# Performance work log

Measured on AMD Instinct MI355X. Metric: run time of the kernel, lower is better.

## Reference

```python
import jax, jax.numpy as jnp
import numpy as np

B, S, D = 1024, 60, 256   # seq_len=60 is hard-coded by nn.Linear(dim*60, n_experts)
H = 1024                  # d_inner
E = 8                     # n_experts
TOPK = 2
CAP = B * TOPK // E       # balanced per-expert capacity = 256


def setup_inputs() -> dict:
    key = jax.random.key(0)
    ks = jax.random.split(key, 9)
    s = 0.02
    return {
        "x":        jax.random.normal(ks[0], (B, S, D), dtype=jnp.float32),
        "W_switch": jax.random.normal(ks[1], (S * D, E), dtype=jnp.float32) * s,
        "b_switch": jnp.zeros((E,), dtype=jnp.float32),
        "W1":       jax.random.normal(ks[2], (E, D, H), dtype=jnp.float32) * s,
        "b1":       jnp.zeros((E, H), dtype=jnp.float32),
        "W2":       jax.random.normal(ks[3], (E, H, D), dtype=jnp.float32) * s,
        "b2":       jnp.zeros((E, D), dtype=jnp.float32),
        "gamma":    jnp.ones((D,), dtype=jnp.float32),
        "beta":     jnp.zeros((D,), dtype=jnp.float32),
    }


def reference(x, W_switch, b_switch, W1, b1, W2, b2, gamma, beta):
    # --- routing: softmax over experts per batch element ---
    logits = x.reshape(B, S * D) @ W_switch + b_switch          # [B, E]
    probs = jax.nn.softmax(logits, axis=-1)
    # balanced dispatch: each expert takes its top-CAP batch indices
    _, idx = jax.lax.top_k(probs.T, CAP)                        # [E, CAP] int32
    xe = x[idx]                                                 # gather -> [E, CAP, S, D]
    # --- per-expert grouped GEMMs (Column- then Row-parallel linear) ---
    h = jax.nn.gelu(jnp.einsum('ecsd,edh->ecsh', xe, W1)
                    + b1[:, None, None, :], approximate=False)  # [E, CAP, S, H]
    oe = jnp.einsum('ecsh,ehd->ecsd', h, W2) + b2[:, None, None, :]  # [E, CAP, S, D]
    # --- scatter-combine via index_add over the batch dim ---
    out = jnp.zeros_like(x).at[idx.reshape(-1)].add(oe.reshape(E * CAP, S, D))
    # --- residual + post-LayerNorm (pre_lnorm=False) ---
    z = x + out
    mu = jnp.mean(z, axis=-1, keepdims=True)
    var = jnp.var(z, axis=-1, keepdims=True)
    return (z - mu) * jax.lax.rsqrt(var + 1e-5) * gamma + beta
```

## Files before the change

kernel.cpp:

```cpp
#include <hip/hip_runtime.h>
#include <hip/hip_bf16.h>
#include <math.h>

#define NB   1024
#define NS   60
#define ND   256
#define NH   1024
#define NE   8
#define NCAP 256
#define NTOK (NCAP*NS)
#define BM   64
#define NBLK (NTOK/BM)
#define A_PAD 264
#define P_PAD 136

typedef __attribute__((ext_vector_type(8))) short  short8;
typedef __attribute__((ext_vector_type(4))) float  floatx4;

__device__ __forceinline__ unsigned short f2bf(float f) {
    union { float f; unsigned u; } cv; cv.f = f;
    unsigned u = cv.u;
    u += 0x7FFFu + ((u >> 16) & 1u);
    return (unsigned short)(u >> 16);
}

__global__ void k_prep_x(const float* __restrict__ x, unsigned short* __restrict__ xb,
                         float* __restrict__ acc, int n4) {
    int i = blockIdx.x * blockDim.x + threadIdx.x;
    if (i >= n4) return;
    float4 v = ((const float4*)x)[i];
    ((float4*)acc)[i] = v;
    ushort4 o;
    o.x = f2bf(v.x); o.y = f2bf(v.y); o.z = f2bf(v.z); o.w = f2bf(v.w);
    ((ushort4*)xb)[i] = o;
}

__global__ void k_pack_w1(const float* __restrict__ W1, unsigned short* __restrict__ W1b) {
    int tid = blockIdx.x * blockDim.x + threadIdx.x;
    int lane = tid & 63;
    int f = tid >> 6;
    int kt  = f & 7;
    int hnt = (f >> 3) & 63;
    int e   = f >> 9;
    int n = hnt * 16 + (lane & 15);
    int k = kt * 32 + (lane >> 4) * 8;
    const float* src = W1 + ((size_t)(e * 256 + k)) * 1024 + n;
    ushort4 a, b;
    a.x = f2bf(src[0 * 1024]); a.y = f2bf(src[1 * 1024]);
    a.z = f2bf(src[2 * 1024]); a.w = f2bf(src[3 * 1024]);
    b.x = f2bf(src[4 * 1024]); b.y = f2bf(src[5 * 1024]);
    b.z = f2bf(src[6 * 1024]); b.w = f2bf(src[7 * 1024]);
    ((ushort4*)W1b)[tid * 2]     = a;
    ((ushort4*)W1b)[tid * 2 + 1] = b;
}

__global__ void k_pack_w2(const float* __restrict__ W2, unsigned short* __restrict__ W2b) {
    int tid = blockIdx.x * blockDim.x + threadIdx.x;
    int lane = tid & 63;
    int f = tid >> 6;
    int kt  = f & 31;
    int dnt = (f >> 5) & 15;
    int e   = f >> 9;
    int n = dnt * 16 + (lane & 15);
    int k = kt * 32 + (lane >> 4) * 8;
    const float* src = W2 + ((size_t)(e * 1024 + k)) * 256 + n;
    ushort4 a, b;
    a.x = f2bf(src[0 * 256]); a.y = f2bf(src[1 * 256]);
    a.z = f2bf(src[2 * 256]); a.w = f2bf(src[3 * 256]);
    b.x = f2bf(src[4 * 256]); b.y = f2bf(src[5 * 256]);
    b.z = f2bf(src[6 * 256]); b.w = f2bf(src[7 * 256]);
    ((ushort4*)W2b)[tid * 2]     = a;
    ((ushort4*)W2b)[tid * 2 + 1] = b;
}

__global__ void k_route(const float* __restrict__ x, const float* __restrict__ Wsw,
                        const float* __restrict__ bsw, float* __restrict__ probs) {
    int b = blockIdx.x;
    int tid = threadIdx.x;
    const float* xr = x + (size_t)b * (NS * ND);
    float a[8];
#pragma unroll
    for (int e = 0; e < 8; ++e) a[e] = 0.f;
    for (int it = 0; it < 60; ++it) {
        int j = tid + it * 256;
        float v = xr[j];
        const float4* w = (const float4*)(Wsw + (size_t)j * 8);
        float4 w0 = w[0], w1 = w[1];
        a[0] += v * w0.x; a[1] += v * w0.y; a[2] += v * w0.z; a[3] += v * w0.w;
        a[4] += v * w1.x; a[5] += v * w1.y; a[6] += v * w1.z; a[7] += v * w1.w;
    }
#pragma unroll
    for (int off = 32; off >= 1; off >>= 1) {
#pragma unroll
        for (int e = 0; e < 8; ++e) a[e] += __shfl_xor(a[e], off);
    }
    __shared__ float red[32];
    __shared__ float ll[8];
    int lane = tid & 63, wv = tid >> 6;
    if (lane == 0) {
#pragma unroll
        for (int e = 0; e < 8; ++e) red[wv * 8 + e] = a[e];
    }
    __syncthreads();
    if (tid < 8) {
        float l = red[0 * 8 + tid] + red[1 * 8 + tid] + red[2 * 8 + tid] + red[3 * 8 + tid]
                + bsw[tid];
        ll[tid] = l;
    }
    __syncthreads();
    if (tid < 8) {
        float m = ll[0];
#pragma unroll
        for (int j = 1; j < 8; ++j) m = fmaxf(m, ll[j]);
        float s = 0.f;
#pragma unroll
        for (int j = 0; j < 8; ++j) s += expf(ll[j] - m);
        probs[b * 8 + tid] = expf(ll[tid] - m) / s;
    }
}

__global__ __launch_bounds__(1024)
void k_topk(const float* __restrict__ probs, int* __restrict__ idxb) {
    __shared__ float v[NB];
    int e = blockIdx.x;
    int tid = threadIdx.x;
    v[tid] = probs[tid * 8 + e];
    __syncthreads();
    float mv = v[tid];
    int cnt = 0;
    for (int j = 0; j < NB; ++j) {
        float vj = v[j];
        cnt += (vj > mv) || (vj == mv && j < tid);
    }
    if (cnt < NCAP) idxb[e * NCAP + cnt] = tid;
}

__global__ __launch_bounds__(256, 2)
void k_mlp(const unsigned short* __restrict__ xb,
           const unsigned short* __restrict__ W1b,
           const unsigned short* __restrict__ W2b,
           const float* __restrict__ b1,
           const float* __restrict__ b2,
           const int* __restrict__ idxb,
           float* __restrict__ acc) {
    __shared__ unsigned short Alds[BM * A_PAD];
    __shared__ unsigned short Plds[BM * P_PAD];

    int e  = blockIdx.x / NBLK;
    int bm = blockIdx.x % NBLK;
    int tb = bm * BM;
    int tid = threadIdx.x;
    int lane = tid & 63, wv = tid >> 6;
    int quad = lane >> 4, l15 = lane & 15;

    {
        int lr = tid >> 2;
        int s4 = tid & 3;
        int t = tb + lr;
        int c = t / 60;
        int s = t - c * 60;
        int bidx = idxb[e * NCAP + c];
        const unsigned short* src = xb + ((size_t)(bidx * 60 + s)) * 256;
#pragma unroll
        for (int j = 0; j < 8; ++j) {
            int seg = j * 4 + s4;
            *(short8*)(&Alds[lr * A_PAD + seg * 8]) = *(const short8*)(src + seg * 8);
        }
    }
    __syncthreads();

    floatx4 acc2[4][4];
#pragma unroll
    for (int mt = 0; mt < 4; ++mt)
#pragma unroll
        for (int nt = 0; nt < 4; ++nt) acc2[mt][nt] = 0.f;

    for (int ch = 0; ch < 8; ++ch) {
        floatx4 pacc[4][2];
#pragma unroll
        for (int mt = 0; mt < 4; ++mt) { pacc[mt][0] = 0.f; pacc[mt][1] = 0.f; }
#pragma unroll
        for (int kt = 0; kt < 8; ++kt) {
            short8 af[4];
#pragma unroll
            for (int mt = 0; mt < 4; ++mt)
                af[mt] = *(const short8*)(&Alds[(mt * 16 + l15) * A_PAD + kt * 32 + quad * 8]);
#pragma unroll
            for (int nt = 0; nt < 2; ++nt) {
                int hnt = ch * 8 + wv * 2 + nt;
                short8 bf = *(const short8*)(W1b + ((size_t)((e * 64 + hnt) * 8 + kt)) * 512 + lane * 8);
#pragma unroll
                for (int mt = 0; mt < 4; ++mt)
                    pacc[mt][nt] = __builtin_amdgcn_mfma_f32_16x16x32_bf16(af[mt], bf, pacc[mt][nt], 0, 0, 0);
            }
        }
        __syncthreads();
#pragma unroll
        for (int nt = 0; nt < 2; ++nt) {
            int cl = wv * 32 + nt * 16 + l15;
            float bias = b1[e * NH + ch * 128 + cl];
#pragma unroll
            for (int mt = 0; mt < 4; ++mt) {
#pragma unroll
                for (int r = 0; r < 4; ++r) {
                    float vv = pacc[mt][nt][r] + bias;
                    float g = 0.5f * vv * (1.0f + erff(vv * 0.70710678118654752f));
                    Plds[(mt * 16 + quad * 4 + r) * P_PAD + cl] = f2bf(g);
                }
            }
        }
        __syncthreads();
#pragma unroll
        for (int kt = 0; kt < 4; ++kt) {
            short8 pf[4];
#pragma unroll
            for (int mt = 0; mt < 4; ++mt)
                pf[mt] = *(const short8*)(&Plds[(mt * 16 + l15) * P_PAD + kt * 32 + quad * 8]);
            int kg = ch * 4 + kt;
#pragma unroll
            for (int nt = 0; nt < 4; ++nt) {
                int dnt = wv * 4 + nt;
                short8 wf = *(const short8*)(W2b + ((size_t)((e * 16 + dnt) * 32 + kg)) * 512 + lane * 8);
#pragma unroll
                for (int mt = 0; mt < 4; ++mt)
                    acc2[mt][nt] = __builtin_amdgcn_mfma_f32_16x16x32_bf16(pf[mt], wf, acc2[mt][nt], 0, 0, 0);
            }
        }
    }

    float b2v[4];
#pragma unroll
    for (int nt = 0; nt < 4; ++nt) b2v[nt] = b2[e * ND + wv * 64 + nt * 16 + l15];
#pragma unroll
    for (int mt = 0; mt < 4; ++mt) {
#pragma unroll
        for (int r = 0; r < 4; ++r) {
            int t = tb + mt * 16 + quad * 4 + r;
            int c = t / 60;
            int s = t - c * 60;
            int bidx = idxb[e * NCAP + c];
            float* dst = acc + ((size_t)(bidx * 60 + s)) * 256 + wv * 64 + l15;
#pragma unroll
            for (int nt = 0; nt < 4; ++nt) {
                unsafeAtomicAdd(dst + nt * 16, acc2[mt][nt][r] + b2v[nt]);
            }
        }
    }
}

__global__ void k_ln(const float* __restrict__ acc, const float* __restrict__ gamma,
                     const float* __restrict__ beta, float* __restrict__ out) {
    int row = blockIdx.x * 4 + (threadIdx.x >> 6);
    int lane = threadIdx.x & 63;
    float4 v = ((const float4*)(acc + (size_t)row * 256))[lane];
    float s = v.x + v.y + v.z + v.w;
    float q = v.x * v.x + v.y * v.y + v.z * v.z + v.w * v.w;
#pragma unroll
    for (int off = 32; off >= 1; off >>= 1) {
        s += __shfl_xor(s, off);
        q += __shfl_xor(q, off);
    }
    float mu  = s * (1.0f / 256.0f);
    float var = q * (1.0f / 256.0f) - mu * mu;
    float rs  = rsqrtf(var + 1e-5f);
    float4 g  = ((const float4*)gamma)[lane];
    float4 bt = ((const float4*)beta)[lane];
    float4 o;
    o.x = (v.x - mu) * rs * g.x + bt.x;
    o.y = (v.y - mu) * rs * g.y + bt.y;
    o.z = (v.z - mu) * rs * g.z + bt.z;
    o.w = (v.w - mu) * rs * g.w + bt.w;
    ((float4*)(out + (size_t)row * 256))[lane] = o;
}

extern "C" void kernel_launch(void* const* d_in, const int* in_sizes, int n_in,
                              void* d_out, int out_size, void* d_ws, size_t ws_size,
                              hipStream_t stream) {
    const float* x     = (const float*)d_in[0];
    const float* Wsw   = (const float*)d_in[1];
    const float* bsw   = (const float*)d_in[2];
    const float* W1    = (const float*)d_in[3];
    const float* b1    = (const float*)d_in[4];
    const float* W2    = (const float*)d_in[5];
    const float* b2    = (const float*)d_in[6];
    const float* gamma = (const float*)d_in[7];
    const float* beta  = (const float*)d_in[8];
    float* out = (float*)d_out;

    char* ws = (char*)d_ws;
    size_t off = 0;
    auto alloc = [&](size_t bytes) { void* p = ws + off; off += (bytes + 255) & ~255ull; return p; };
    float*          probs = (float*)alloc((size_t)NB * NE * 4);
    int*            idxb  = (int*)alloc((size_t)NE * NCAP * 4);
    unsigned short* xb    = (unsigned short*)alloc((size_t)NB * NS * ND * 2);
    unsigned short* W1b   = (unsigned short*)alloc((size_t)NE * ND * NH * 2);
    unsigned short* W2b   = (unsigned short*)alloc((size_t)NE * NH * ND * 2);
    float*          acc   = (float*)alloc((size_t)NB * NS * ND * 4);
    (void)ws_size; (void)in_sizes; (void)n_in; (void)out_size;

    int n4 = NB * NS * ND / 4;
    k_prep_x<<<(n4 + 255) / 256, 256, 0, stream>>>(x, xb, acc, n4);
    k_pack_w1<<<1024, 256, 0, stream>>>(W1, W1b);
    k_pack_w2<<<1024, 256, 0, stream>>>(W2, W2b);
    k_route<<<NB, 256, 0, stream>>>(x, Wsw, bsw, probs);
    k_topk<<<NE, 1024, 0, stream>>>(probs, idxb);
    k_mlp<<<NE * NBLK, 256, 0, stream>>>(xb, W1b, W2b, b1, b2, idxb, acc);
    k_ln<<<NB * NS / 4, 256, 0, stream>>>(acc, gamma, beta, out);
}
```

Baseline: 465.7 us.

## Fuse x conversion into routing, replace atomic scatter with gather-combine in LayerNorm

Folds the x-to-bf16 conversion into a split routing kernel that writes per-slice partial logits, and moves softmax into a parallelised top-k that also records per-batch slot lists. The MLP kernel now writes bf16 expert outputs to a buffer instead of atomically adding fp32 into an accumulator. LayerNorm gathers those outputs per row, which removes the atomics and the accumulator copy of x. Weight packing switches to coalesced float4 reads, the MLP uses a tanh-form GELU with a fast exp and occupancy 3, and P_PAD changes. The exact erf GELU is replaced by an approximation and the expert outputs are stored in bf16, both of which cost accuracy.

```diff
diff --git a/kernel.cpp b/kernel.cpp
--- a/kernel.cpp
+++ b/kernel.cpp
@@ -12,9 +12,10 @@
 #define BM   64
 #define NBLK (NTOK/BM)
 #define A_PAD 264
-#define P_PAD 136
+#define P_PAD 132
 
 typedef __attribute__((ext_vector_type(8))) short  short8;
+typedef __attribute__((ext_vector_type(4))) short  s4v;
 typedef __attribute__((ext_vector_type(4))) float  floatx4;
 
 __device__ __forceinline__ unsigned short f2bf(float f) {
@@ -23,131 +24,145 @@
     u += 0x7FFFu + ((u >> 16) & 1u);
     return (unsigned short)(u >> 16);
 }
-
-__global__ void k_prep_x(const float* __restrict__ x, unsigned short* __restrict__ xb,
-                         float* __restrict__ acc, int n4) {
-    int i = blockIdx.x * blockDim.x + threadIdx.x;
-    if (i >= n4) return;
-    float4 v = ((const float4*)x)[i];
-    ((float4*)acc)[i] = v;
-    ushort4 o;
-    o.x = f2bf(v.x); o.y = f2bf(v.y); o.z = f2bf(v.z); o.w = f2bf(v.w);
-    ((ushort4*)xb)[i] = o;
+__device__ __forceinline__ float bf2f(unsigned short h) {
+    union { unsigned u; float f; } c; c.u = ((unsigned)h) << 16; return c.f;
 }
 
 __global__ void k_pack_w1(const float* __restrict__ W1, unsigned short* __restrict__ W1b) {
-    int tid = blockIdx.x * blockDim.x + threadIdx.x;
-    int lane = tid & 63;
-    int f = tid >> 6;
-    int kt  = f & 7;
-    int hnt = (f >> 3) & 63;
-    int e   = f >> 9;
-    int n = hnt * 16 + (lane & 15);
-    int k = kt * 32 + (lane >> 4) * 8;
-    const float* src = W1 + ((size_t)(e * 256 + k)) * 1024 + n;
-    ushort4 a, b;
-    a.x = f2bf(src[0 * 1024]); a.y = f2bf(src[1 * 1024]);
-    a.z = f2bf(src[2 * 1024]); a.w = f2bf(src[3 * 1024]);
-    b.x = f2bf(src[4 * 1024]); b.y = f2bf(src[5 * 1024]);
-    b.z = f2bf(src[6 * 1024]); b.w = f2bf(src[7 * 1024]);
-    ((ushort4*)W1b)[tid * 2]     = a;
-    ((ushort4*)W1b)[tid * 2 + 1] = b;
+    int idx = blockIdx.x * 256 + threadIdx.x;
+    int n4 = idx & 255;
+    int k  = (idx >> 8) & 255;
+    int e  = idx >> 16;
+    int n  = n4 * 4;
+    float4 w = *(const float4*)(W1 + ((size_t)(e * 256 + k)) * 1024 + n);
+    int f = (e * 64 + (n >> 4)) * 8 + (k >> 5);
+    int L = ((k >> 3) & 3) * 16 + (n & 15);
+    int j = k & 7;
+    unsigned short* dst = W1b + (size_t)f * 512 + L * 8 + j;
+    dst[0]  = f2bf(w.x);
+    dst[8]  = f2bf(w.y);
+    dst[16] = f2bf(w.z);
+    dst[24] = f2bf(w.w);
 }
 
 __global__ void k_pack_w2(const float* __restrict__ W2, unsigned short* __restrict__ W2b) {
-    int tid = blockIdx.x * blockDim.x + threadIdx.x;
-    int lane = tid & 63;
-    int f = tid >> 6;
-    int kt  = f & 31;
-    int dnt = (f >> 5) & 15;
-    int e   = f >> 9;
-    int n = dnt * 16 + (lane & 15);
-    int k = kt * 32 + (lane >> 4) * 8;
-    const float* src = W2 + ((size_t)(e * 1024 + k)) * 256 + n;
-    ushort4 a, b;
-    a.x = f2bf(src[0 * 256]); a.y = f2bf(src[1 * 256]);
-    a.z = f2bf(src[2 * 256]); a.w = f2bf(src[3 * 256]);
-    b.x = f2bf(src[4 * 256]); b.y = f2bf(src[5 * 256]);
-    b.z = f2bf(src[6 * 256]); b.w = f2bf(src[7 * 256]);
-    ((ushort4*)W2b)[tid * 2]     = a;
-    ((ushort4*)W2b)[tid * 2 + 1] = b;
-}
-
-__global__ void k_route(const float* __restrict__ x, const float* __restrict__ Wsw,
-                        const float* __restrict__ bsw, float* __restrict__ probs) {
-    int b = blockIdx.x;
+    int idx = blockIdx.x * 256 + threadIdx.x;
+    int d4 = idx & 63;
+    int h  = (idx >> 6) & 1023;
+    int e  = idx >> 16;
+    int d  = d4 * 4;
+    float4 w = *(const float4*)(W2 + ((size_t)(e * 1024 + h)) * 256 + d);
+    int f = (e * 16 + (d >> 4)) * 32 + (h >> 5);
+    int L = ((h >> 3) & 3) * 16 + (d & 15);
+    int j = h & 7;
+    unsigned short* dst = W2b + (size_t)f * 512 + L * 8 + j;
+    dst[0]  = f2bf(w.x);
+    dst[8]  = f2bf(w.y);
+    dst[16] = f2bf(w.z);
+    dst[24] = f2bf(w.w);
+}
+
+__global__ __launch_bounds__(256)
+void k_route(const float* __restrict__ x, const float* __restrict__ Wsw,
+             unsigned short* __restrict__ xb, float* __restrict__ partials) {
+    int g = blockIdx.x & 127;
+    int s = blockIdx.x >> 7;
+    int team = threadIdx.x >> 5;
+    int j = threadIdx.x & 31;
+    int b = g * 8 + team;
+    const float* xr = x + (size_t)b * 15360 + s * 1920;
+    unsigned short* xbr = xb + (size_t)b * 15360 + s * 1920;
+    float a[8];
+#pragma unroll
+    for (int e = 0; e < 8; ++e) a[e] = 0.f;
+    for (int it = 0; it < 15; ++it) {
+        int k = it * 128 + j * 4;
+        float4 xv = *(const float4*)(xr + k);
+        ushort4 o;
+        o.x = f2bf(xv.x); o.y = f2bf(xv.y); o.z = f2bf(xv.z); o.w = f2bf(xv.w);
+        *(ushort4*)(xbr + k) = o;
+        float xa[4] = {xv.x, xv.y, xv.z, xv.w};
+        const float* w = Wsw + (size_t)(s * 1920 + k) * 8;
+#pragma unroll
+        for (int c = 0; c < 4; ++c) {
+            float4 w0 = *(const float4*)(w + c * 8);
+            float4 w1 = *(const float4*)(w + c * 8 + 4);
+            float xc = xa[c];
+            a[0] += xc * w0.x; a[1] += xc * w0.y; a[2] += xc * w0.z; a[3] += xc * w0.w;
+            a[4] += xc * w1.x; a[5] += xc * w1.y; a[6] += xc * w1.z; a[7] += xc * w1.w;
+        }
+    }
+#pragma unroll
+    for (int m = 16; m >= 1; m >>= 1) {
+#pragma unroll
+        for (int e = 0; e < 8; ++e) a[e] += __shfl_xor(a[e], m);
+    }
+    if (j == 0) {
+        float4* p = (float4*)(partials + ((size_t)(s * 1024) + b) * 8);
+        p[0] = make_float4(a[0], a[1], a[2], a[3]);
+        p[1] = make_float4(a[4], a[5], a[6], a[7]);
+    }
+}
+
+__global__ __launch_bounds__(256)
+void k_topk(const float* __restrict__ partials, const float* __restrict__ bsw,
+            int* __restrict__ idxb, int* __restrict__ cntb, int* __restrict__ slotb) {
+    __shared__ float v[NB];
+    int e = blockIdx.x >> 2;
+    int q = blockIdx.x & 3;
     int tid = threadIdx.x;
-    const float* xr = x + (size_t)b * (NS * ND);
-    float a[8];
-#pragma unroll
-    for (int e = 0; e < 8; ++e) a[e] = 0.f;
-    for (int it = 0; it < 60; ++it) {
-        int j = tid + it * 256;
-        float v = xr[j];
-        const float4* w = (const float4*)(Wsw + (size_t)j * 8);
-        float4 w0 = w[0], w1 = w[1];
-        a[0] += v * w0.x; a[1] += v * w0.y; a[2] += v * w0.z; a[3] += v * w0.w;
-        a[4] += v * w1.x; a[5] += v * w1.y; a[6] += v * w1.z; a[7] += v * w1.w;
-    }
-#pragma unroll
-    for (int off = 32; off >= 1; off >>= 1) {
-#pragma unroll
-        for (int e = 0; e < 8; ++e) a[e] += __shfl_xor(a[e], off);
-    }
-    __shared__ float red[32];
-    __shared__ float ll[8];
-    int lane = tid & 63, wv = tid >> 6;
-    if (lane == 0) {
-#pragma unroll
-        for (int e = 0; e < 8; ++e) red[wv * 8 + e] = a[e];
+    float bs[8];
+#pragma unroll
+    for (int i = 0; i < 8; ++i) bs[i] = bsw[i];
+#pragma unroll
+    for (int rr = 0; rr < 4; ++rr) {
+        int row = rr * 256 + tid;
+        float l[8];
+#pragma unroll
+        for (int i = 0; i < 8; ++i) l[i] = bs[i];
+#pragma unroll
+        for (int s = 0; s < 8; ++s) {
+            const float4* p = (const float4*)(partials + ((size_t)(s * 1024) + row) * 8);
+            float4 p0 = p[0], p1 = p[1];
+            l[0] += p0.x; l[1] += p0.y; l[2] += p0.z; l[3] += p0.w;
+            l[4] += p1.x; l[5] += p1.y; l[6] += p1.z; l[7] += p1.w;
+        }
+        float m = l[0];
+#pragma unroll
+        for (int i = 1; i < 8; ++i) m = fmaxf(m, l[i]);
+        float sum = 0.f;
+#pragma unroll
+        for (int i = 0; i < 8; ++i) sum += expf(l[i] - m);
+        v[row] = expf(l[e] - m) / sum;
     }
     __syncthreads();
-    if (tid < 8) {
-        float l = red[0 * 8 + tid] + red[1 * 8 + tid] + red[2 * 8 + tid] + red[3 * 8 + tid]
-                + bsw[tid];
-        ll[tid] = l;
-    }
-    __syncthreads();
-    if (tid < 8) {
-        float m = ll[0];
-#pragma unroll
-        for (int j = 1; j < 8; ++j) m = fmaxf(m, ll[j]);
-        float s = 0.f;
-#pragma unroll
-        for (int j = 0; j < 8; ++j) s += expf(ll[j] - m);
-        probs[b * 8 + tid] = expf(ll[tid] - m) / s;
-    }
-}
-
-__global__ __launch_bounds__(1024)
-void k_topk(const float* __restrict__ probs, int* __restrict__ idxb) {
-    __shared__ float v[NB];
-    int e = blockIdx.x;
-    int tid = threadIdx.x;
-    v[tid] = probs[tid * 8 + e];
-    __syncthreads();
-    float mv = v[tid];
+    int cand = q * 256 + tid;
+    float mv = v[cand];
     int cnt = 0;
-    for (int j = 0; j < NB; ++j) {
-        float vj = v[j];
-        cnt += (vj > mv) || (vj == mv && j < tid);
-    }
-    if (cnt < NCAP) idxb[e * NCAP + cnt] = tid;
-}
-
-__global__ __launch_bounds__(256, 2)
+    for (int jj = 0; jj < NB; ++jj) {
+        float vj = v[jj];
+        cnt += (vj > mv) || (vj == mv && jj < cand);
+    }
+    if (cnt < NCAP) {
+        idxb[e * NCAP + cnt] = cand;
+        int pos = atomicAdd(&cntb[cand], 1);
+        slotb[cand * 8 + pos] = e * NCAP + cnt;
+    }
+}
+
+__global__ __launch_bounds__(256, 3)
 void k_mlp(const unsigned short* __restrict__ xb,
            const unsigned short* __restrict__ W1b,
            const unsigned short* __restrict__ W2b,
            const float* __restrict__ b1,
            const float* __restrict__ b2,
            const int* __restrict__ idxb,
-           float* __restrict__ acc) {
-    __shared__ unsigned short Alds[BM * A_PAD];
-    __shared__ unsigned short Plds[BM * P_PAD];
-
-    int e  = blockIdx.x / NBLK;
-    int bm = blockIdx.x % NBLK;
+           unsigned short* __restrict__ oe) {
+    __shared__ __align__(16) unsigned short Alds[BM * A_PAD];
+    __shared__ __align__(16) unsigned short Plds[BM * P_PAD];
+
+    int e  = blockIdx.x & 7;
+    int bm = blockIdx.x >> 3;
     int tb = bm * BM;
     int tid = threadIdx.x;
     int lane = tid & 63, wv = tid >> 6;
@@ -204,7 +219,9 @@
 #pragma unroll
                 for (int r = 0; r < 4; ++r) {
                     float vv = pacc[mt][nt][r] + bias;
-                    float g = 0.5f * vv * (1.0f + erff(vv * 0.70710678118654752f));
+                    float t2 = vv * vv;
+                    float z = vv * fmaf(t2, -0.0713548162726f, -1.5957691216057308f);
+                    float g = vv * __builtin_amdgcn_rcpf(1.0f + __expf(z));
                     Plds[(mt * 16 + quad * 4 + r) * P_PAD + cl] = f2bf(g);
                 }
             }
@@ -214,8 +231,12 @@
         for (int kt = 0; kt < 4; ++kt) {
             short8 pf[4];
 #pragma unroll
-            for (int mt = 0; mt < 4; ++mt)
-                pf[mt] = *(const short8*)(&Plds[(mt * 16 + l15) * P_PAD + kt * 32 + quad * 8]);
+            for (int mt = 0; mt < 4; ++mt) {
+                const unsigned short* pb = &Plds[(mt * 16 + l15) * P_PAD + kt * 32 + quad * 8];
+                s4v p0 = *(const s4v*)(pb);
+                s4v p1 = *(const s4v*)(pb + 4);
+                pf[mt] = __builtin_shufflevector(p0, p1, 0, 1, 2, 3, 4, 5, 6, 7);
+            }
             int kg = ch * 4 + kt;
 #pragma unroll
             for (int nt = 0; nt < 4; ++nt) {
@@ -236,31 +257,38 @@
 #pragma unroll
         for (int r = 0; r < 4; ++r) {
             int t = tb + mt * 16 + quad * 4 + r;
-            int c = t / 60;
-            int s = t - c * 60;
-            int bidx = idxb[e * NCAP + c];
-            float* dst = acc + ((size_t)(bidx * 60 + s)) * 256 + wv * 64 + l15;
-#pragma unroll
-            for (int nt = 0; nt < 4; ++nt) {
-                unsafeAtomicAdd(dst + nt * 16, acc2[mt][nt][r] + b2v[nt]);
-            }
-        }
-    }
-}
-
-__global__ void k_ln(const float* __restrict__ acc, const float* __restrict__ gamma,
-                     const float* __restrict__ beta, float* __restrict__ out) {
+            unsigned short* dst = oe + ((size_t)(e * NTOK + t)) * 256 + wv * 64 + l15;
+#pragma unroll
+            for (int nt = 0; nt < 4; ++nt)
+                dst[nt * 16] = f2bf(acc2[mt][nt][r] + b2v[nt]);
+        }
+    }
+}
+
+__global__ void k_ln(const float* __restrict__ x, const unsigned short* __restrict__ oe,
+                     const int* __restrict__ cntb, const int* __restrict__ slotb,
+                     const float* __restrict__ gamma, const float* __restrict__ beta,
+                     float* __restrict__ out) {
     int row = blockIdx.x * 4 + (threadIdx.x >> 6);
     int lane = threadIdx.x & 63;
-    float4 v = ((const float4*)(acc + (size_t)row * 256))[lane];
-    float s = v.x + v.y + v.z + v.w;
+    int b = row / 60;
+    int s = row - b * 60;
+    float4 v = ((const float4*)(x + (size_t)row * 256))[lane];
+    int cnt = cntb[b];
+    const int* sl = slotb + b * 8;
+    for (int i = 0; i < cnt; ++i) {
+        int slot = sl[i];
+        ushort4 ov = ((const ushort4*)(oe + ((size_t)slot * 60 + s) * 256))[lane];
+        v.x += bf2f(ov.x); v.y += bf2f(ov.y); v.z += bf2f(ov.z); v.w += bf2f(ov.w);
+    }
+    float sm = v.x + v.y + v.z + v.w;
     float q = v.x * v.x + v.y * v.y + v.z * v.z + v.w * v.w;
 #pragma unroll
     for (int off = 32; off >= 1; off >>= 1) {
-        s += __shfl_xor(s, off);
-        q += __shfl_xor(q, off);
-    }
-    float mu  = s * (1.0f / 256.0f);
+        sm += __shfl_xor(sm, off);
+        q  += __shfl_xor(q, off);
+    }
+    float mu  = sm * (1.0f / 256.0f);
     float var = q * (1.0f / 256.0f) - mu * mu;
     float rs  = rsqrtf(var + 1e-5f);
     float4 g  = ((const float4*)gamma)[lane];
@@ -290,20 +318,21 @@
     char* ws = (char*)d_ws;
     size_t off = 0;
     auto alloc = [&](size_t bytes) { void* p = ws + off; off += (bytes + 255) & ~255ull; return p; };
-    float*          probs = (float*)alloc((size_t)NB * NE * 4);
-    int*            idxb  = (int*)alloc((size_t)NE * NCAP * 4);
-    unsigned short* xb    = (unsigned short*)alloc((size_t)NB * NS * ND * 2);
-    unsigned short* W1b   = (unsigned short*)alloc((size_t)NE * ND * NH * 2);
-    unsigned short* W2b   = (unsigned short*)alloc((size_t)NE * NH * ND * 2);
-    float*          acc   = (float*)alloc((size_t)NB * NS * ND * 4);
+    float*          partials = (float*)alloc((size_t)8 * NB * NE * 4);
+    int*            idxb     = (int*)alloc((size_t)NE * NCAP * 4);
+    int*            cntb     = (int*)alloc((size_t)NB * 4);
+    int*            slotb    = (int*)alloc((size_t)NB * 8 * 4);
+    unsigned short* xb       = (unsigned short*)alloc((size_t)NB * NS * ND * 2);
+    unsigned short* W1b      = (unsigned short*)alloc((size_t)NE * ND * NH * 2);
+    unsigned short* W2b      = (unsigned short*)alloc((size_t)NE * NH * ND * 2);
+    unsigned short* oe       = (unsigned short*)alloc((size_t)NE * NTOK * ND * 2);
     (void)ws_size; (void)in_sizes; (void)n_in; (void)out_size;
 
-    int n4 = NB * NS * ND / 4;
-    k_prep_x<<<(n4 + 255) / 256, 256, 0, stream>>>(x, xb, acc, n4);
-    k_pack_w1<<<1024, 256, 0, stream>>>(W1, W1b);
-    k_pack_w2<<<1024, 256, 0, stream>>>(W2, W2b);
-    k_route<<<NB, 256, 0, stream>>>(x, Wsw, bsw, probs);
-    k_topk<<<NE, 1024, 0, stream>>>(probs, idxb);
-    k_mlp<<<NE * NBLK, 256, 0, stream>>>(xb, W1b, W2b, b1, b2, idxb, acc);
-    k_ln<<<NB * NS / 4, 256, 0, stream>>>(acc, gamma, beta, out);
-}
+    hipMemsetAsync(cntb, 0, (size_t)NB * 4, stream);
+    k_route<<<1024, 256, 0, stream>>>(x, Wsw, xb, partials);
+    k_pack_w1<<<2048, 256, 0, stream>>>(W1, W1b);
+    k_pack_w2<<<2048, 256, 0, stream>>>(W2, W2b);
+    k_topk<<<32, 256, 0, stream>>>(partials, bsw, idxb, cntb, slotb);
+    k_mlp<<<NE * NBLK, 256, 0, stream>>>(xb, W1b, W2b, b1, b2, idxb, oe);
+    k_ln<<<NB * NS / 4, 256, 0, stream>>>(x, oe, cntb, slotb, gamma, beta, out);
+}
```

New measurement: 508.8 us. +9.3%, slower.
